# Optimization experiments

Measured on AMD Instinct MI355X. Metric: run time of the kernel, lower is better.

Reference implementation:

```python
import jax, jax.numpy as jnp
import numpy as np

# MyConvT config (matches init_kwargs)
K, S, P, OP = 5, 2, 2, 1  # kernel, stride, padding, output_padding


def setup_inputs() -> dict:
    key = jax.random.key(0)
    k0, k1, k2, k3 = jax.random.split(key, 4)
    B, Cin, Cout, H, W = 8, 192, 128, 64, 64
    OH = (H - 1) * S + K - 2 * P + OP  # 128
    OW = (W - 1) * S + K - 2 * P + OP  # 128
    x = jax.random.normal(k0, (B, Cin, H, W), jnp.float32)
    # mask spatial must be (OH + K - 1, OW + K - 1) so its unfold has OH*OW columns
    mask = jax.random.randint(k1, (B, 1, OH + K - 1, OW + K - 1), 0, 2, jnp.int32)
    # torch ConvTranspose2d weight layout: [in_channels, out_channels, kH, kW]
    weight = jax.random.normal(k2, (Cin, Cout, K, K), jnp.float32) * 0.05
    bias = jax.random.normal(k3, (Cout,), jnp.float32) * 0.05
    return {"x": x, "mask": mask, "weight": weight, "bias": bias}


def _masked_conv_transpose(x, mask, weight, bias):
    # The torch module does: zero-insert (stride dilation), pad (K-1-P each side,
    # plus OP trailing), unfold, gather valid patches (where the unfolded mask
    # patch has any nonzero), dense matmul with rot180/transposed weight + bias,
    # then masked_scatter back (zeros elsewhere). Mathematically:
    #   out = mask_any * (conv_transpose2d(x, weight) + bias)
    # where mask_any[b,oh,ow] = any(mask[b,:, oh:oh+K, ow:ow+K] != 0).
    kern = jnp.flip(weight, (2, 3)).transpose(1, 0, 2, 3)  # -> OIHW correlation kernel
    pad = ((K - 1 - P, K - 1 - P + OP), (K - 1 - P, K - 1 - P + OP))
    y = jax.lax.conv_general_dilated(
        x, kern, window_strides=(1, 1), padding=pad, lhs_dilation=(S, S),
        dimension_numbers=("NCHW", "OIHW", "NCHW"))  # [B, Cout, OH, OW]
    m = (mask != 0).astype(y.dtype)  # [B, 1, OH+K-1, OW+K-1]
    pooled = jax.lax.reduce_window(m, 0.0, jax.lax.max,
                                   (1, 1, K, K), (1, 1, 1, 1), "VALID")  # [B,1,OH,OW]
    return jnp.where(pooled > 0, y + bias[None, :, None, None], 0.0)


def reference(x, mask, weight, bias):
    return _masked_conv_transpose(x, mask, weight, bias)
```

## Files before the change

kernel.cpp:

```cpp
#include <hip/hip_runtime.h>


#define NB   8
#define CIN  192
#define COUT 128
#define HH   64
#define OHH  128
#define OWW  128
#define MH   132
#define MW   132

#define X4_IYH_B 27648
#define PLANE_B  9216
#define XBUF_B   36864
#define WOFF     36864
#define NSLOT    5
#define LDS_B    (XBUF_B + NSLOT * 8192)

typedef short bf16x8 __attribute__((ext_vector_type(8)));
typedef float f32x4  __attribute__((ext_vector_type(4)));
typedef float f32x2  __attribute__((ext_vector_type(2)));

static __device__ __forceinline__ unsigned short f2bf(float f) {
  union { float f; unsigned int u; } a; a.f = f;
  return (unsigned short)((a.u + 0x7fffu + ((a.u >> 16) & 1u)) >> 16);
}

#define GLOAD_LDS16(gp, lp) __builtin_amdgcn_global_load_lds(                      \
    (const __attribute__((address_space(1))) void*)(gp),                           \
    (__attribute__((address_space(3))) void*)(lp), 16, 0, 0)

__global__ __launch_bounds__(256) void prep_k(
    const float* __restrict__ x, const int* __restrict__ mask,
    const float* __restrict__ w, unsigned short* __restrict__ x4,
    unsigned short* __restrict__ w4, unsigned char* __restrict__ many) {
  const int bid = blockIdx.x, tid = threadIdx.x;

  if (bid < 528) {
    const int b = bid / 66, iyH = bid % 66;
    const int lane = tid & 63, wv = tid >> 6;
    unsigned short* pl = x4 + (size_t)(b * 66 + iyH) * (X4_IYH_B / 2);

    if (iyH == 0 || iyH == 65) {
      for (int i = tid; i < X4_IYH_B / 16; i += 256)
        *(uint4*)(pl + i * 8) = make_uint4(0, 0, 0, 0);
      return;
    }
    const int iy = iyH - 1;
    if (tid < 48) {
      int c3 = tid >> 4, rr = (tid >> 3) & 1, ch = tid & 7;
      *(uint4*)(pl + (c3 * 72 + rr * 65) * 64 + ch * 8) = make_uint4(0, 0, 0, 0);
    }
    #pragma unroll
    for (int k = 0; k < 6; ++k) {
      int ci0 = wv * 48 + k * 8;
      int c3 = ci0 >> 6, cr = ci0 & 63;
      unsigned short p[8];
      #pragma unroll
      for (int e = 0; e < 8; ++e)
        p[e] = f2bf(x[(((size_t)b * CIN + ci0 + e) * HH + iy) * HH + lane]);
      uint4 v;
      v.x = (unsigned)p[0] | ((unsigned)p[1] << 16);
      v.y = (unsigned)p[2] | ((unsigned)p[3] << 16);
      v.z = (unsigned)p[4] | ((unsigned)p[5] << 16);
      v.w = (unsigned)p[6] | ((unsigned)p[7] << 16);
      *(uint4*)(pl + ((size_t)c3 * 72 + 1 + lane) * 64 + cr) = v;
    }
  } else if (bid < 624) {
    int idx = (bid - 528) * 256 + tid;
    int ci = idx % CIN, co = idx / CIN;
    int cob = co >> 6, c = co & 63, c3 = ci >> 6, cir = ci & 63;
    const float* src = w + (size_t)(ci * COUT + co) * 25;
    #pragma unroll
    for (int tap = 0; tap < 25; ++tap)
      w4[(size_t)((tap * 2 + cob) * 3 + c3) * 4096 + c * 64 + cir] = f2bf(src[tap]);
  } else {
    int g = (bid - 624) * 256 + tid;
    int owq = g & 31, oh = (g >> 5) & 127, b = g >> 12;
    const int* mp = mask + (b * MH + oh) * MW + owq * 4;
    int a0 = 0, a1 = 0, a2 = 0, a3 = 0;
    #pragma unroll
    for (int i = 0; i < 5; ++i) {
      int4 u = *(const int4*)(mp + i * MW);
      int4 v = *(const int4*)(mp + i * MW + 4);
      int c = u.z | u.w | v.x;
      a0 |= u.x | u.y | c;
      a1 |= u.y | c | v.y;
      a2 |= c | v.y | v.z;
      a3 |= u.w | v.x | v.y | v.z | v.w;
    }
    *(uchar4*)(many + ((size_t)b * OHH + oh) * OWW + owq * 4) =
        make_uchar4(a0 ? 1 : 0, a1 ? 1 : 0, a2 ? 1 : 0, a3 ? 1 : 0);
  }
}

__constant__ const int TKH[25] = {0,0,1,1, 0,0,1,1, 0,1, 2,2,3,3, 2,2,3,3, 2,3, 4,4, 4,4, 4};
__constant__ const int TKW[25] = {0,1,0,1, 2,3,2,3, 4,4, 0,1,0,1, 2,3,2,3, 4,4, 0,1, 2,3, 4};

#define BF_LOAD(S, KK, KJ)                                                     \
  { const int p_ = oyr + 2 - (KK);                                             \
    _Pragma("unroll") for (int k2 = 0; k2 < 2; ++k2)                           \
      _Pragma("unroll") for (int ti = 0; ti < 4; ++ti) {                       \
        const int row_ = ti * 16 + l15 + 2 - (KJ);                             \
        bfr[S][k2][ti] = *(const bf16x8*)(lds + p_ * PLANE_B + row_ * 128 +    \
                                          (((k2 * 4 + kc) ^ (row_ & 7)) << 4)); } }

#define AF_LOAD(T)                                                             \
  { const char* ws_ = lds + WOFF + ((T) % 5) * 8192;                           \
    _Pragma("unroll") for (int k2 = 0; k2 < 2; ++k2)                           \
      _Pragma("unroll") for (int mi = 0; mi < 2; ++mi) {                       \
        const int row_ = cos * 32 + mi * 16 + l15;                             \
        afr[k2][mi] = *(const bf16x8*)(ws_ + row_ * 128 +                      \
                                       (((k2 * 4 + kc) ^ (l15 & 7)) << 4)); } }

#define SG(T)                                                                  \
  { if (c3 < 2 || (T) < 22) {                                                  \
      const int tn_ = ((T) + 3 < 25) ? (T) + 3 : (T) - 22;                     \
      const int cn_ = ((T) + 3 < 25) ? c3 : c3 + 1;                            \
      stage_w(TKH[tn_] * 5 + TKW[tn_], cn_, ((T) + 3) % 5);                    \
    }                                                                          \
    if (c3 == 2 && (T) >= 22) {                                                \
      if ((T) == 22)      asm volatile("s_waitcnt vmcnt(4)" ::: "memory");     \
      else if ((T) == 23) asm volatile("s_waitcnt vmcnt(2)" ::: "memory");     \
      else                asm volatile("s_waitcnt vmcnt(0)" ::: "memory");     \
    } else {                                                                   \
      asm volatile("s_waitcnt vmcnt(6)" ::: "memory");                         \
    }                                                                          \
    __builtin_amdgcn_s_barrier(); }

#define MM(S, PH_, PW_)                                                        \
  { __builtin_amdgcn_s_setprio(1);                                             \
    _Pragma("unroll") for (int k2 = 0; k2 < 2; ++k2)                           \
      _Pragma("unroll") for (int mi = 0; mi < 2; ++mi)                         \
        _Pragma("unroll") for (int ti = 0; ti < 4; ++ti)                       \
          acc[PH_][PW_][mi][ti] = __builtin_amdgcn_mfma_f32_16x16x32_bf16(     \
              afr[k2][mi], bfr[S][k2][ti], acc[PH_][PW_][mi][ti], 0, 0, 0);    \
    __builtin_amdgcn_s_setprio(0); }

#define TAP(T, PH_, PW_, S)        { SG(T) AF_LOAD(T) MM(S, PH_, PW_) }
#define TAPP(T, PH_, PW_, S, KK, KJ) \
  { SG(T) AF_LOAD(T) BF_LOAD((S) ^ 1, KK, KJ) MM(S, PH_, PW_) }

__global__ __launch_bounds__(256, 2) void convt_mfma(
    const unsigned short* __restrict__ x4, const unsigned short* __restrict__ w4,
    const float* __restrict__ bias, const unsigned char* __restrict__ many,
    float* __restrict__ out) {
  __shared__ __align__(16) char lds[LDS_B];

  const int tid = threadIdx.x, lane = tid & 63, wv = tid >> 6;
  const int l15 = lane & 15, kc = lane >> 4;
  const int cos = wv & 1, oyr = wv >> 1;
  const int b = blockIdx.x & 7, qq = blockIdx.x >> 3;
  const int cob = qq & 1, oyq = qq >> 1;
  const int oy0 = oyq * 2, oy = oy0 + oyr;
  const int sswz = (lane >> 3) * 128 + (((lane & 7) ^ (lane >> 3)) << 4);

  const char* x4b = (const char*)x4 + (size_t)(b * 66 + oy0) * X4_IYH_B;
  const char* w4b = (const char*)w4 + cob * 24576;

  f32x4 acc[2][2][2][4];
  #pragma unroll
  for (int p = 0; p < 2; ++p)
    #pragma unroll
    for (int q2 = 0; q2 < 2; ++q2)
      #pragma unroll
      for (int i = 0; i < 2; ++i)
        #pragma unroll
        for (int j = 0; j < 4; ++j)
          acc[p][q2][i][j] = (f32x4){0.f, 0.f, 0.f, 0.f};

  auto stage_x = [&](int c3) {
    #pragma unroll
    for (int j = 0; j < 9; ++j) {
      int qc = wv + 4 * j;
      int p = qc / 9, ch = qc % 9;
      GLOAD_LDS16(x4b + (size_t)p * X4_IYH_B + c3 * PLANE_B + ch * 1024 + sswz,
                  lds + p * PLANE_B + ch * 1024 + lane * 16);
    }
  };
  auto stage_w = [&](int tapid, int c3n, int slot) {
    const char* s = w4b + (size_t)tapid * 49152 + c3n * 8192 + wv * 2048 + sswz;
    char* d = lds + WOFF + slot * 8192 + wv * 2048 + lane * 16;
    GLOAD_LDS16(s, d);
    GLOAD_LDS16(s + 1024, d + 1024);
  };

  stage_x(0);
  stage_w(0, 0, 0);
  stage_w(1, 0, 1);
  stage_w(5, 0, 2);
  asm volatile("s_waitcnt vmcnt(4)" ::: "memory");
  __builtin_amdgcn_s_barrier();

  bf16x8 bfr[2][2][4], afr[2][2];
  #pragma unroll 1
  for (int c3 = 0; c3 < 3; ++c3) {
    BF_LOAD(0, 0, 0)
    TAP (0,  0, 0, 0) TAP (1,  0, 1, 0) TAP (2,  1, 0, 0)
    TAPP(3,  1, 1, 0, 0, 1)
    TAP (4,  0, 0, 1) TAP (5,  0, 1, 1) TAP (6,  1, 0, 1)
    TAPP(7,  1, 1, 1, 0, 2)
    TAP (8,  0, 0, 0)
    TAPP(9,  1, 0, 0, 1, 0)
    TAP (10, 0, 0, 1) TAP (11, 0, 1, 1) TAP (12, 1, 0, 1)
    TAPP(13, 1, 1, 1, 1, 1)
    TAP (14, 0, 0, 0) TAP (15, 0, 1, 0) TAP (16, 1, 0, 0)
    TAPP(17, 1, 1, 0, 1, 2)
    TAP (18, 0, 0, 1)
    TAPP(19, 1, 0, 1, 2, 0)
    TAP (20, 0, 0, 0)
    TAPP(21, 0, 1, 0, 2, 1)
    TAP (22, 0, 0, 1)
    TAPP(23, 0, 1, 1, 2, 2)
    TAP (24, 0, 0, 0)
    if (c3 < 2) {
      __builtin_amdgcn_s_barrier();
      stage_x(c3 + 1);
      asm volatile("s_waitcnt vmcnt(0)" ::: "memory");
      __builtin_amdgcn_s_barrier();
    }
  }

  const int cobase = cob * 64 + cos * 32;
  #pragma unroll
  for (int mi = 0; mi < 2; ++mi) {
    const f32x4 bv = *(const f32x4*)(bias + cobase + mi * 16 + kc * 4);
    #pragma unroll
    for (int ph = 0; ph < 2; ++ph) {
      const int oh = 2 * oy + ph;
      const unsigned char* mrow = many + ((size_t)b * OHH + oh) * OWW;
      #pragma unroll
      for (int ti = 0; ti < 4; ++ti) {
        const int ow0 = 2 * (ti * 16 + l15);
        const unsigned short m2 = *(const unsigned short*)(mrow + ow0);
        #pragma unroll
        for (int r = 0; r < 4; ++r) {
          const int co = cobase + mi * 16 + kc * 4 + r;
          f32x2 v;
          v.x = (m2 & 0x00FFu) ? acc[ph][0][mi][ti][r] + bv[r] : 0.f;
          v.y = (m2 & 0xFF00u) ? acc[ph][1][mi][ti][r] + bv[r] : 0.f;
          *(f32x2*)(out + (((size_t)(b * COUT + co)) * OHH + oh) * OWW + ow0) = v;
        }
      }
    }
  }
}

extern "C" void kernel_launch(void* const* d_in, const int* in_sizes, int n_in,
                              void* d_out, int out_size, void* d_ws, size_t ws_size,
                              hipStream_t stream) {
  const float* x    = (const float*)d_in[0];
  const int*   mask = (const int*)d_in[1];
  const float* w    = (const float*)d_in[2];
  const float* bias = (const float*)d_in[3];
  float* out = (float*)d_out;

  unsigned char*  many = (unsigned char*)d_ws;
  unsigned short* x4   = (unsigned short*)((char*)d_ws + 131072);
  unsigned short* w4   = (unsigned short*)((char*)d_ws + 131072 +
                                           (size_t)NB * 66 * X4_IYH_B);

  prep_k<<<752, 256, 0, stream>>>(x, mask, w, x4, w4, many);
  convt_mfma<<<512, 256, 0, stream>>>(x4, w4, bias, many, out);
}
```

Measured before the change: 61.08 us.

## Process weight taps in pairs per barrier and single-buffer B fragments

Restructures the per-channel-chunk tap loop so each barrier step stages two weight taps ahead and runs two taps' MFMAs. This roughly halves the number of workgroup barriers and vmcnt waits per chunk. The B-fragment register double buffer becomes a single buffer, while A fragments become double-buffered across the pair, which changes register pressure. The tap order is remapped through a constexpr table. Prefetching two slots ahead inside a five-slot ring shortens the reuse distance, which risks a write-after-read race on the slot read in the previous pair.

```diff
diff --git a/kernel.cpp b/kernel.cpp
--- a/kernel.cpp
+++ b/kernel.cpp
@@ -94,58 +94,59 @@
   }
 }
 
-__constant__ const int TKH[25] = {0,0,1,1, 0,0,1,1, 0,1, 2,2,3,3, 2,2,3,3, 2,3, 4,4, 4,4, 4};
-__constant__ const int TKW[25] = {0,1,0,1, 2,3,2,3, 4,4, 0,1,0,1, 2,3,2,3, 4,4, 0,1, 2,3, 4};
-
-#define BF_LOAD(S, KK, KJ)                                                     \
+
+#define VMC(N) asm volatile("s_waitcnt vmcnt(" #N ")" ::: "memory")
+
+#define GATE(T)                                                                \
+  { if ((T) == 24 && c3 == 2)      VMC(0);                                     \
+    else if ((T) == 22 && c3 == 2) VMC(2);                                     \
+    else                           VMC(6);                                     \
+    __builtin_amdgcn_s_barrier(); }
+
+#define BF_LOAD(KK, KJ)                                                        \
   { const int p_ = oyr + 2 - (KK);                                             \
     _Pragma("unroll") for (int k2 = 0; k2 < 2; ++k2)                           \
       _Pragma("unroll") for (int ti = 0; ti < 4; ++ti) {                       \
         const int row_ = ti * 16 + l15 + 2 - (KJ);                             \
-        bfr[S][k2][ti] = *(const bf16x8*)(lds + p_ * PLANE_B + row_ * 128 +    \
-                                          (((k2 * 4 + kc) ^ (row_ & 7)) << 4)); } }
-
-#define AF_LOAD(T)                                                             \
+        bfr[k2][ti] = *(const bf16x8*)(lds + p_ * PLANE_B + row_ * 128 +       \
+                                       (((k2 * 4 + kc) ^ (row_ & 7)) << 4)); } }
+
+#define AF_LOADJ(J, T)                                                         \
   { const char* ws_ = lds + WOFF + ((T) % 5) * 8192;                           \
     _Pragma("unroll") for (int k2 = 0; k2 < 2; ++k2)                           \
       _Pragma("unroll") for (int mi = 0; mi < 2; ++mi) {                       \
         const int row_ = cos * 32 + mi * 16 + l15;                             \
-        afr[k2][mi] = *(const bf16x8*)(ws_ + row_ * 128 +                      \
-                                       (((k2 * 4 + kc) ^ (l15 & 7)) << 4)); } }
-
-#define SG(T)                                                                  \
-  { if (c3 < 2 || (T) < 22) {                                                  \
-      const int tn_ = ((T) + 3 < 25) ? (T) + 3 : (T) - 22;                     \
-      const int cn_ = ((T) + 3 < 25) ? c3 : c3 + 1;                            \
-      stage_w(TKH[tn_] * 5 + TKW[tn_], cn_, ((T) + 3) % 5);                    \
-    }                                                                          \
-    if (c3 == 2 && (T) >= 22) {                                                \
-      if ((T) == 22)      asm volatile("s_waitcnt vmcnt(4)" ::: "memory");     \
-      else if ((T) == 23) asm volatile("s_waitcnt vmcnt(2)" ::: "memory");     \
-      else                asm volatile("s_waitcnt vmcnt(0)" ::: "memory");     \
-    } else {                                                                   \
-      asm volatile("s_waitcnt vmcnt(6)" ::: "memory");                         \
-    }                                                                          \
-    __builtin_amdgcn_s_barrier(); }
-
-#define MM(S, PH_, PW_)                                                        \
+        afr[J][k2][mi] = *(const bf16x8*)(ws_ + row_ * 128 +                   \
+                                          (((k2 * 4 + kc) ^ (l15 & 7)) << 4)); } }
+
+#define MMJ(J, PH_, PW_)                                                       \
   { __builtin_amdgcn_s_setprio(1);                                             \
     _Pragma("unroll") for (int k2 = 0; k2 < 2; ++k2)                           \
       _Pragma("unroll") for (int mi = 0; mi < 2; ++mi)                         \
         _Pragma("unroll") for (int ti = 0; ti < 4; ++ti)                       \
           acc[PH_][PW_][mi][ti] = __builtin_amdgcn_mfma_f32_16x16x32_bf16(     \
-              afr[k2][mi], bfr[S][k2][ti], acc[PH_][PW_][mi][ti], 0, 0, 0);    \
+              afr[J][k2][mi], bfr[k2][ti], acc[PH_][PW_][mi][ti], 0, 0, 0);    \
     __builtin_amdgcn_s_setprio(0); }
 
-#define TAP(T, PH_, PW_, S)        { SG(T) AF_LOAD(T) MM(S, PH_, PW_) }
-#define TAPP(T, PH_, PW_, S, KK, KJ) \
-  { SG(T) AF_LOAD(T) BF_LOAD((S) ^ 1, KK, KJ) MM(S, PH_, PW_) }
+#define PAIRB(T, KK, KJ, PH0, PW0, PH1, PW1)                                   \
+  { stage_u((T) + 3); stage_u((T) + 4); GATE(T)                                \
+    BF_LOAD(KK, KJ) AF_LOADJ(0, T) AF_LOADJ(1, (T) + 1)                        \
+    MMJ(0, PH0, PW0) MMJ(1, PH1, PW1) }
+#define PAIRN(T, PH0, PW0, PH1, PW1)                                           \
+  { stage_u((T) + 3); stage_u((T) + 4); GATE(T)                                \
+    AF_LOADJ(0, T) AF_LOADJ(1, (T) + 1)                                        \
+    MMJ(0, PH0, PW0) MMJ(1, PH1, PW1) }
+#define PH1B(T, KK, KJ, PH0, PW0)                                              \
+  { stage_u((T) + 3); GATE(T)                                                  \
+    BF_LOAD(KK, KJ) AF_LOADJ(0, T) MMJ(0, PH0, PW0) }
 
 __global__ __launch_bounds__(256, 2) void convt_mfma(
     const unsigned short* __restrict__ x4, const unsigned short* __restrict__ w4,
     const float* __restrict__ bias, const unsigned char* __restrict__ many,
     float* __restrict__ out) {
   __shared__ __align__(16) char lds[LDS_B];
+  constexpr int TID[25] = {0,1,5,6, 2,3,7,8, 4,9, 10,11,15,16, 12,13,17,18,
+                           14,19, 20,21, 22,23, 24};
 
   const int tid = threadIdx.x, lane = tid & 63, wv = tid >> 6;
   const int l15 = lane & 15, kc = lane >> 4;
@@ -184,39 +185,37 @@
     GLOAD_LDS16(s, d);
     GLOAD_LDS16(s + 1024, d + 1024);
   };
+  int c3 = 0;
+  auto stage_u = [&](int u) {
+    if (u <= 24) stage_w(TID[u], c3, u % 5);
+    else if (c3 < 2) stage_w(TID[u - 25], c3 + 1, (u - 25) % 5);
+  };
 
   stage_x(0);
-  stage_w(0, 0, 0);
-  stage_w(1, 0, 1);
-  stage_w(5, 0, 2);
-  asm volatile("s_waitcnt vmcnt(4)" ::: "memory");
-  __builtin_amdgcn_s_barrier();
-
-  bf16x8 bfr[2][2][4], afr[2][2];
+  stage_w(TID[0], 0, 0);
+  stage_w(TID[1], 0, 1);
+  stage_w(TID[2], 0, 2);
+
+  bf16x8 bfr[2][4], afr[2][2][2];
   #pragma unroll 1
-  for (int c3 = 0; c3 < 3; ++c3) {
-    BF_LOAD(0, 0, 0)
-    TAP (0,  0, 0, 0) TAP (1,  0, 1, 0) TAP (2,  1, 0, 0)
-    TAPP(3,  1, 1, 0, 0, 1)
-    TAP (4,  0, 0, 1) TAP (5,  0, 1, 1) TAP (6,  1, 0, 1)
-    TAPP(7,  1, 1, 1, 0, 2)
-    TAP (8,  0, 0, 0)
-    TAPP(9,  1, 0, 0, 1, 0)
-    TAP (10, 0, 0, 1) TAP (11, 0, 1, 1) TAP (12, 1, 0, 1)
-    TAPP(13, 1, 1, 1, 1, 1)
-    TAP (14, 0, 0, 0) TAP (15, 0, 1, 0) TAP (16, 1, 0, 0)
-    TAPP(17, 1, 1, 0, 1, 2)
-    TAP (18, 0, 0, 1)
-    TAPP(19, 1, 0, 1, 2, 0)
-    TAP (20, 0, 0, 0)
-    TAPP(21, 0, 1, 0, 2, 1)
-    TAP (22, 0, 0, 1)
-    TAPP(23, 0, 1, 1, 2, 2)
-    TAP (24, 0, 0, 0)
+  for (c3 = 0; c3 < 3; ++c3) {
+    PAIRB(0,  0, 0,  0, 0,  0, 1)
+    PAIRN(2,         1, 0,  1, 1)
+    PAIRB(4,  0, 1,  0, 0,  0, 1)
+    PAIRN(6,         1, 0,  1, 1)
+    PAIRB(8,  0, 2,  0, 0,  1, 0)
+    PAIRB(10, 1, 0,  0, 0,  0, 1)
+    PAIRN(12,        1, 0,  1, 1)
+    PAIRB(14, 1, 1,  0, 0,  0, 1)
+    PAIRN(16,        1, 0,  1, 1)
+    PAIRB(18, 1, 2,  0, 0,  1, 0)
+    PAIRB(20, 2, 0,  0, 0,  0, 1)
+    PAIRB(22, 2, 1,  0, 0,  0, 1)
+    PH1B (24, 2, 2,  0, 0)
     if (c3 < 2) {
       __builtin_amdgcn_s_barrier();
       stage_x(c3 + 1);
-      asm volatile("s_waitcnt vmcnt(0)" ::: "memory");
+      VMC(0);
       __builtin_amdgcn_s_barrier();
     }
   }
```

Result: faster. 55.12 us (-9.8%).
